# Optimization experiments

Hardware: AMD Instinct MI355X
Metric: run time of the kernel (lower is better)

Reference implementation:

```python
import jax, jax.numpy as jnp
import numpy as np

N_QUBITS = 20
W_MUL = (2.0 ** 0.5) * (5.0 ** -0.5)  # he_std = gain * 5**-0.5, use_wscale=True, lrmul=1

_C = jnp.complex64
X = jnp.array([[0, 1], [1, 0]], dtype=_C)
Y = jnp.array([[0, -1j], [1j, 0]], dtype=_C)
Z = jnp.array([[1, 0], [0, -1]], dtype=_C)
I2 = jnp.eye(2, dtype=_C)
I4 = jnp.eye(4, dtype=_C)
XX = jnp.kron(X, X)
YY = jnp.kron(Y, Y)
ZZ = jnp.kron(Z, Z)


def _rot(theta, pauli, ident):
    # exp(-i * theta/2 * P) = cos(theta/2) I - i sin(theta/2) P
    a = theta * 0.5
    return jnp.cos(a) * ident - (1j * jnp.sin(a)) * pauli


def _apply_1q(state, g, w):
    # state: [batch] + [2]*n ; contract gate input index with qubit axis w
    s = jnp.tensordot(g, state, axes=((1,), (w + 1,)))
    return jnp.moveaxis(s, 0, w + 1)


def _apply_2q(state, g4, w0, w1):
    g = g4.reshape(2, 2, 2, 2)  # (out0, out1, in0, in1)
    s = jnp.tensordot(g, state, axes=((2, 3), (w0 + 1, w1 + 1)))
    return jnp.moveaxis(s, (0, 1), (w0 + 1, w1 + 1))


def _xyz_layer(psi, params, n):
    # params: [3n]; rx, ry, rz on each wire
    for q in range(n):
        psi = _apply_1q(psi, _rot(params[3 * q], X, I2), q)
        psi = _apply_1q(psi, _rot(params[3 * q + 1], Y, I2), q)
        psi = _apply_1q(psi, _rot(params[3 * q + 2], Z, I2), q)
    return psi


def _circuit(psi, w, n):
    psi = _xyz_layer(psi, w[: 3 * n], n)
    for q in range(n - 1):
        i = 3 * n + 3 * q
        psi = _apply_2q(psi, _rot(w[i], XX, I4), q, q + 1)
        psi = _apply_2q(psi, _rot(w[i + 1], YY, I4), q, q + 1)
        psi = _apply_2q(psi, _rot(w[i + 2], ZZ, I4), q, q + 1)
    psi = _xyz_layer(psi, w[6 * n - 3 :], n)
    return psi


def setup_inputs() -> dict:
    key = jax.random.key(0)
    k1, k2 = jax.random.split(key)
    n = N_QUBITS
    dim = 1 << n
    batch = 4
    x = jax.random.normal(k1, (batch, 1, dim), dtype=jnp.float32)
    weight = jax.random.uniform(k2, (9 * n - 3,), dtype=jnp.float32, minval=0.0, maxval=2.0 * np.pi)
    return {"x": x, "weight": weight, "dimA": 10}


def reference(x, weight, dimA):
    n = N_QUBITS
    batch = x.shape[0]
    w = weight * W_MUL
    psi = x.astype(_C).reshape((batch,) + (2,) * n)  # MPS tensor [b, 2, ..., 2]
    psi = _circuit(psi, w, n)
    dimB = n - dimA
    # partial trace of |psi><psi| over the first dimB qubits (most-significant axes):
    # reduced[a, c] = sum_t psi[t, a] * conj(psi[t, c])  -- never materialize the full DM
    psi = psi.reshape(batch, 1 << dimB, 1 << dimA)
    rdm = jnp.einsum('bta,btc->bac', psi, psi.conj())
    # return real/imag stacked on last axis (real-valued representation of complex DM)
    return jnp.stack([rdm.real, rdm.imag], axis=-1)
```

## Files before the change

kernel.cpp:

```cpp
#include <hip/hip_runtime.h>
#include <hip/hip_bf16.h>

#define N_Q    20
#define DIM    (1 << N_Q)
#define BATCH  4
#define NGATES 19
#define L2OFF  117
#define GSTRIDE 32

typedef float2 c32;
typedef __attribute__((ext_vector_type(2))) float fv2;
typedef __attribute__((ext_vector_type(8))) short short8;
typedef __attribute__((ext_vector_type(4))) float f32x4;
typedef __attribute__((ext_vector_type(4))) unsigned int u32x4;

__device__ __forceinline__ c32 cmul(c32 a, c32 b) {
    return make_float2(fmaf(a.x, b.x, -a.y * b.y), fmaf(a.x, b.y, a.y * b.x));
}
__device__ __forceinline__ c32 cmadd(c32 acc, c32 a, c32 b) {
    acc.x = fmaf(a.x, b.x, fmaf(-a.y, b.y, acc.x));
    acc.y = fmaf(a.x, b.y, fmaf(a.y, b.x, acc.y));
    return acc;
}
__device__ __forceinline__ unsigned short f2bf(float f) {
    union { float f; unsigned u; } v; v.f = f;
    unsigned r = v.u + 0x7FFFu + ((v.u >> 16) & 1u);
    return (unsigned short)(r >> 16);
}
__device__ __forceinline__ unsigned pack_bf2(float re, float im) {
    return (unsigned)f2bf(re) | ((unsigned)f2bf(im) << 16);
}
__device__ __forceinline__ fv2 unpack_bf2(unsigned w) {
    union { unsigned u; float f; } lo, hi;
    lo.u = (w & 0xFFFFu) << 16;
    hi.u = w & 0xFFFF0000u;
    return (fv2){lo.f, hi.f};
}
__device__ __forceinline__ void gll16(const void* g, void* l) {
    __builtin_amdgcn_global_load_lds((const __attribute__((address_space(1))) void*)g,
                                     (__attribute__((address_space(3))) void*)l, 16, 0, 0);
}

__device__ void mm2(const c32 A[2][2], const c32 B[2][2], c32 C[2][2]) {
    for (int i = 0; i < 2; i++)
        for (int j = 0; j < 2; j++) {
            c32 s = make_float2(0.f, 0.f);
            for (int k = 0; k < 2; k++) s = cmadd(s, A[i][k], B[k][j]);
            C[i][j] = s;
        }
}
__device__ void mm4(const c32 A[4][4], const c32 B[4][4], c32 C[4][4]) {
    for (int i = 0; i < 4; i++)
        for (int j = 0; j < 4; j++) {
            c32 s = make_float2(0.f, 0.f);
            for (int k = 0; k < 4; k++) s = cmadd(s, A[i][k], B[k][j]);
            C[i][j] = s;
        }
}
__device__ void single_u(const float* w, int base, c32 U[2][2]) {
    const float WM = 0.63245553203367586640f;
    float hx = w[base] * WM * 0.5f, hy = w[base + 1] * WM * 0.5f, hz = w[base + 2] * WM * 0.5f;
    float cx = cosf(hx), sx = sinf(hx);
    float cy = cosf(hy), sy = sinf(hy);
    float cz = cosf(hz), sz = sinf(hz);
    c32 RX[2][2] = {{{cx, 0.f}, {0.f, -sx}}, {{0.f, -sx}, {cx, 0.f}}};
    c32 RY[2][2] = {{{cy, 0.f}, {-sy, 0.f}}, {{sy, 0.f}, {cy, 0.f}}};
    c32 RZ[2][2] = {{{cz, -sz}, {0.f, 0.f}}, {{0.f, 0.f}, {cz, sz}}};
    c32 T[2][2];
    mm2(RY, RX, T);
    mm2(RZ, T, U);
}
__device__ void kron22(const c32 A[2][2], const c32 B[2][2], c32 K[4][4]) {
    for (int i = 0; i < 2; i++)
        for (int j = 0; j < 2; j++)
            for (int k = 0; k < 2; k++)
                for (int l = 0; l < 2; l++)
                    K[i * 2 + j][k * 2 + l] = cmul(A[i][k], B[j][l]);
}

__global__ void build_gates(const float* __restrict__ w, c32* __restrict__ G) {
    int q = threadIdx.x;
    if (q >= NGATES) return;
    const float WM = 0.63245553203367586640f;
    float hx = w[60 + 3 * q] * WM * 0.5f;
    float hy = w[61 + 3 * q] * WM * 0.5f;
    float hz = w[62 + 3 * q] * WM * 0.5f;
    float cx = cosf(hx), sx = sinf(hx);
    float cy = cosf(hy), sy = sinf(hy);
    float cz = cosf(hz), sz = sinf(hz);
    c32 RXX[4][4], RYY[4][4], RZZ[4][4];
    for (int i = 0; i < 4; i++)
        for (int j = 0; j < 4; j++) {
            RXX[i][j] = make_float2(0.f, 0.f);
            RYY[i][j] = make_float2(0.f, 0.f);
            RZZ[i][j] = make_float2(0.f, 0.f);
        }
    for (int i = 0; i < 4; i++) {
        RXX[i][i]     = make_float2(cx, 0.f);
        RXX[i][3 - i] = make_float2(0.f, -sx);
        RYY[i][i]     = make_float2(cy, 0.f);
    }
    RYY[0][3] = make_float2(0.f,  sy);
    RYY[1][2] = make_float2(0.f, -sy);
    RYY[2][1] = make_float2(0.f, -sy);
    RYY[3][0] = make_float2(0.f,  sy);
    RZZ[0][0] = make_float2(cz, -sz);
    RZZ[1][1] = make_float2(cz,  sz);
    RZZ[2][2] = make_float2(cz,  sz);
    RZZ[3][3] = make_float2(cz, -sz);
    c32 T[4][4], M[4][4];
    mm4(RYY, RXX, T);
    mm4(RZZ, T, M);

    c32 I2m[2][2] = {{{1.f, 0.f}, {0.f, 0.f}}, {{0.f, 0.f}, {1.f, 0.f}}};
    c32 Ua[2][2], Ub[2][2], Pre[4][4], Post[4][4];
    if (q == 0) {
        single_u(w, 0, Ua);
        single_u(w, 3, Ub);
        kron22(Ua, Ub, Pre);
    } else {
        single_u(w, 3 * (q + 1), Ub);
        kron22(I2m, Ub, Pre);
    }
    if (q == NGATES - 1) {
        single_u(w, L2OFF + 3 * 18, Ua);
        single_u(w, L2OFF + 3 * 19, Ub);
        kron22(Ua, Ub, Post);
    } else {
        single_u(w, L2OFF + 3 * q, Ua);
        kron22(Ua, I2m, Post);
    }
    c32 T2[4][4], Gq[4][4];
    mm4(M, Pre, T2);
    mm4(Post, T2, Gq);
    for (int i = 0; i < 4; i++)
        for (int j = 0; j < 4; j++) {
            c32 g = Gq[i][j];
            G[q * GSTRIDE + i * 4 + j]      = g;
            G[q * GSTRIDE + 16 + i * 4 + j] = make_float2(-g.y, g.x);
        }
}

__device__ __forceinline__ void apply4pk(const fv2 g[16], const fv2 gs[16],
                                         fv2& x0, fv2& x1, fv2& x2, fv2& x3) {
    fv2 a0 = (fv2)(x0[0]), b0 = (fv2)(x0[1]);
    fv2 a1 = (fv2)(x1[0]), b1 = (fv2)(x1[1]);
    fv2 a2 = (fv2)(x2[0]), b2 = (fv2)(x2[1]);
    fv2 a3 = (fv2)(x3[0]), b3 = (fv2)(x3[1]);
    fv2 r0 = a0 * g[0];  r0 += b0 * gs[0];  r0 += a1 * g[1];  r0 += b1 * gs[1];
    r0 += a2 * g[2];     r0 += b2 * gs[2];  r0 += a3 * g[3];  r0 += b3 * gs[3];
    fv2 r1 = a0 * g[4];  r1 += b0 * gs[4];  r1 += a1 * g[5];  r1 += b1 * gs[5];
    r1 += a2 * g[6];     r1 += b2 * gs[6];  r1 += a3 * g[7];  r1 += b3 * gs[7];
    fv2 r2 = a0 * g[8];  r2 += b0 * gs[8];  r2 += a1 * g[9];  r2 += b1 * gs[9];
    r2 += a2 * g[10];    r2 += b2 * gs[10]; r2 += a3 * g[11]; r2 += b3 * gs[11];
    fv2 r3 = a0 * g[12]; r3 += b0 * gs[12]; r3 += a1 * g[13]; r3 += b1 * gs[13];
    r3 += a2 * g[14];    r3 += b2 * gs[14]; r3 += a3 * g[15]; r3 += b3 * gs[15];
    x0 = r0; x1 = r1; x2 = r2; x3 = r3;
}
__device__ __forceinline__ void load_gate2(const fv2* __restrict__ gp, fv2 g[16], fv2 gs[16]) {
#pragma unroll
    for (int k = 0; k < 16; k++) { g[k] = gp[k]; gs[k] = gp[16 + k]; }
}
template <int LO>
__device__ __forceinline__ void gate_on32(fv2 v[32], const fv2 g[16], const fv2 gs[16]) {
#pragma unroll
    for (int m = 0; m < 8; ++m) {
        const int j0 = ((m >> LO) << (LO + 2)) | (m & ((1 << LO) - 1));
        const int s = 1 << LO;
        apply4pk(g, gs, v[j0], v[j0 + s], v[j0 + 2 * s], v[j0 + 3 * s]);
    }
}
template <int LO>
__device__ __forceinline__ void gate_on16(fv2* v, const fv2 g[16], const fv2 gs[16]) {
#pragma unroll
    for (int m = 0; m < 4; ++m) {
        const int j0 = ((m >> LO) << (LO + 2)) | (m & ((1 << LO) - 1));
        const int s = 1 << LO;
        apply4pk(g, gs, v[j0], v[j0 + s], v[j0 + 2 * s], v[j0 + 3 * s]);
    }
}

#define SIDX(l) ((l) ^ ((((l) >> 5) & 15)))
#define TIDX(a, tl) (((a) << 3) | ((tl) ^ (((a) >> 5) & 7)))

__global__ __launch_bounds__(256) void pass_a2(const float* __restrict__ x,
                                               unsigned* __restrict__ psiB,
                                               const c32* __restrict__ Gall) {
    __shared__ __align__(16) char smem[65536];
    float* xs = (float*)smem;
    fv2* s = (fv2*)smem;
    const fv2* Gf = (const fv2*)Gall;
    int b = blockIdx.x >> 7;
    int c0 = (blockIdx.x & 127) << 5;
    const float* xp = x + ((size_t)b << 20) + c0;
    unsigned* ppb = psiB + ((size_t)b << 20) + c0;
    int t = threadIdx.x;
#pragma unroll
    for (int i = 0; i < 8; ++i) {
        int f4 = t + (i << 8);
        int row = f4 >> 3, sl = f4 & 7;
        float4 v = *reinterpret_cast<const float4*>(xp + (size_t)row * 4096 + sl * 4);
        reinterpret_cast<float4*>(xs)[row * 8 + (sl ^ (row & 7))] = v;
    }
    __syncthreads();
    int col = t & 31, rlow = t >> 5;
    fv2 v[32], g[16], gs[16];
#pragma unroll
    for (int j = 0; j < 32; ++j) {
        int row = (j << 3) | rlow;
        float re = xs[row * 32 + ((((col >> 2) ^ (row & 7)) << 2) | (col & 3))];
        v[j] = (fv2){re, 0.f};
    }
    __syncthreads();
    load_gate2(Gf + 0 * GSTRIDE, g, gs);  gate_on32<3>(v, g, gs);
    load_gate2(Gf + 1 * GSTRIDE, g, gs);  gate_on32<2>(v, g, gs);
    load_gate2(Gf + 2 * GSTRIDE, g, gs);  gate_on32<1>(v, g, gs);
    load_gate2(Gf + 3 * GSTRIDE, g, gs);  gate_on32<0>(v, g, gs);
#pragma unroll
    for (int j = 0; j < 32; ++j) {
        int l = ((((j << 3) | rlow) << 5)) | col;
        s[SIDX(l)] = v[j];
    }
    __syncthreads();
    int rhi = t >> 5;
#pragma unroll
    for (int rtop = 0; rtop < 2; ++rtop)
#pragma unroll
        for (int j = 0; j < 16; ++j) {
            int row = (rtop << 7) | (rhi << 4) | j;
            int l = (row << 5) | col;
            v[rtop * 16 + j] = s[SIDX(l)];
        }
    load_gate2(Gf + 4 * GSTRIDE, g, gs);  gate_on16<2>(v, g, gs);  gate_on16<2>(v + 16, g, gs);
    load_gate2(Gf + 5 * GSTRIDE, g, gs);  gate_on16<1>(v, g, gs);  gate_on16<1>(v + 16, g, gs);
    load_gate2(Gf + 6 * GSTRIDE, g, gs);  gate_on16<0>(v, g, gs);  gate_on16<0>(v + 16, g, gs);
#pragma unroll
    for (int rtop = 0; rtop < 2; ++rtop)
#pragma unroll
        for (int j = 0; j < 16; ++j) {
            int row = (rtop << 7) | (rhi << 4) | j;
            fv2 val = v[rtop * 16 + j];
            ppb[(size_t)row * 4096 + col] = pack_bf2(val[0], val[1]);
        }
}

__global__ __launch_bounds__(256) void pass_b2(const unsigned* __restrict__ psiB,
                                               unsigned short* __restrict__ Art,
                                               unsigned short* __restrict__ Ait,
                                               const c32* __restrict__ Gall) {
    __shared__ fv2 s[8192];
    const fv2* Gf = (const fv2*)Gall;
    int b = blockIdx.x >> 7;
    int chunk = blockIdx.x & 127;
    const unsigned* ppb = psiB + ((size_t)b << 20) + ((size_t)chunk << 13);
    int t = threadIdx.x;
    fv2 v[32], g[16], gs[16];
#pragma unroll
    for (int j = 0; j < 32; ++j) v[j] = unpack_bf2(ppb[(j << 8) | t]);
    load_gate2(Gf + 7 * GSTRIDE, g, gs);   gate_on32<3>(v, g, gs);
    load_gate2(Gf + 8 * GSTRIDE, g, gs);   gate_on32<2>(v, g, gs);
    load_gate2(Gf + 9 * GSTRIDE, g, gs);   gate_on32<1>(v, g, gs);
    load_gate2(Gf + 10 * GSTRIDE, g, gs);  gate_on32<0>(v, g, gs);
#pragma unroll
    for (int j = 0; j < 32; ++j) { int l = (j << 8) | t; s[SIDX(l)] = v[j]; }
    __syncthreads();
    int hi2 = (t >> 4) << 9, lo2 = t & 15;
#pragma unroll
    for (int j = 0; j < 32; ++j) { int l = hi2 | (j << 4) | lo2; v[j] = s[SIDX(l)]; }
    load_gate2(Gf + 11 * GSTRIDE, g, gs);  gate_on32<3>(v, g, gs);
    load_gate2(Gf + 12 * GSTRIDE, g, gs);  gate_on32<2>(v, g, gs);
    load_gate2(Gf + 13 * GSTRIDE, g, gs);  gate_on32<1>(v, g, gs);
    load_gate2(Gf + 14 * GSTRIDE, g, gs);  gate_on32<0>(v, g, gs);
    __syncthreads();
#pragma unroll
    for (int j = 0; j < 32; ++j) { int l = hi2 | (j << 4) | lo2; s[SIDX(l)] = v[j]; }
    __syncthreads();
#pragma unroll
    for (int j = 0; j < 32; ++j) { int l = (t << 5) | j; v[j] = s[SIDX(l)]; }
    load_gate2(Gf + 15 * GSTRIDE, g, gs);  gate_on32<3>(v, g, gs);
    load_gate2(Gf + 16 * GSTRIDE, g, gs);  gate_on32<2>(v, g, gs);
    load_gate2(Gf + 17 * GSTRIDE, g, gs);  gate_on32<1>(v, g, gs);
    load_gate2(Gf + 18 * GSTRIDE, g, gs);  gate_on32<0>(v, g, gs);
    __syncthreads();
    {
        int tlw = t >> 5;
        int abase = (t & 31) << 5;
#pragma unroll
        for (int j = 0; j < 32; ++j) {
            int a = abase + j;
            s[TIDX(a, tlw)] = v[j];
        }
    }
    __syncthreads();
    {
        int w = t >> 6, lane = t & 63;
        size_t gb = (size_t)b << 20;
#pragma unroll
        for (int i = 0; i < 4; ++i) {
            int a = (w << 8) | (i << 6) | lane;
            unsigned short rr[8], ri[8];
#pragma unroll
            for (int tl = 0; tl < 8; ++tl) {
                fv2 q = s[TIDX(a, tl)];
                rr[tl] = f2bf(q[0]);
                ri[tl] = f2bf(q[1]);
            }
            size_t dst = gb + ((size_t)a << 10) + (chunk << 3);
            *reinterpret_cast<float4*>(Art + dst) = *reinterpret_cast<float4*>(rr);
            *reinterpret_cast<float4*>(Ait + dst) = *reinterpret_cast<float4*>(ri);
        }
    }
}

__global__ __launch_bounds__(512) void gram_mfma5c(const unsigned short* __restrict__ Art,
                                                   const unsigned short* __restrict__ Ait,
                                                   float2* __restrict__ out) {
    __shared__ __align__(16) unsigned short lds[2][4][8192];
    int hw = blockIdx.x;
    int virt = (hw & 7) * 18 + (hw >> 3);
    int b = virt / 36;
    int rem = virt - b * 36;
    int ia = 0;
    while (rem >= 8 - ia) { rem -= 8 - ia; ++ia; }
    int ic = ia + rem;
    int a0 = ia * 128, c0 = ic * 128;
    int tid = threadIdx.x;
    int lane = tid & 63, w = tid >> 6;
    int wm = w & 3, wn = w >> 2;
    int arr = w >> 1, half = w & 1;
    const unsigned short* sp = (arr & 1) ? Ait : Art;
    int prow = (arr < 2) ? a0 : c0;
    int srow = lane >> 3, sslot = lane & 7;
    size_t gb = (size_t)b << 20;

    f32x4 accRe[2][4], accIm[2][4];
#pragma unroll
    for (int m = 0; m < 2; m++)
#pragma unroll
        for (int n = 0; n < 4; n++) { accRe[m][n] = (f32x4)0.f; accIm[m][n] = (f32x4)0.f; }

#define STAGE5(KT, BUF)                                                                   \
    {                                                                                     \
        _Pragma("unroll")                                                                 \
        for (int i = 0; i < 8; ++i) {                                                     \
            int r = (half << 6) | (i << 3) | srow;                                        \
            int sl = sslot ^ srow;                                                        \
            const unsigned short* gp = sp + gb + ((size_t)(prow + r) << 10) + (KT) * 64 + sl * 8; \
            gll16(gp, &lds[BUF][arr][((half << 6) | (i << 3)) * 64 + lane * 8]);          \
        }                                                                                 \
    }

    STAGE5(0, 0);
    for (int kt = 0; kt < 16; ++kt) {
        int cur = kt & 1;
        asm volatile("s_waitcnt vmcnt(0)" ::: "memory");
        __builtin_amdgcn_s_barrier();
        __builtin_amdgcn_sched_barrier(0);
        if (kt < 15) STAGE5(kt + 1, cur ^ 1);
        __builtin_amdgcn_s_setprio(1);
#pragma unroll
        for (int kk = 0; kk < 2; ++kk) {
            int sbase = kk * 4 + (lane >> 4);
            short8 am[2][2], bn[4][2];
#pragma unroll
            for (int m = 0; m < 2; m++) {
                int r = wm * 32 + m * 16 + (lane & 15);
                int off = r * 64 + ((sbase ^ (r & 7)) << 3);
                am[m][0] = *reinterpret_cast<const short8*>(&lds[cur][0][off]);
                am[m][1] = *reinterpret_cast<const short8*>(&lds[cur][1][off]);
            }
#pragma unroll
            for (int n = 0; n < 4; n++) {
                int r = wn * 64 + n * 16 + (lane & 15);
                int off = r * 64 + ((sbase ^ (r & 7)) << 3);
                bn[n][0] = *reinterpret_cast<const short8*>(&lds[cur][2][off]);
                bn[n][1] = *reinterpret_cast<const short8*>(&lds[cur][3][off]);
            }
#pragma unroll
            for (int m = 0; m < 2; m++) {
                u32x4 tn = *reinterpret_cast<u32x4*>(&am[m][0]) ^ 0x80008000u;
                short8 arn = *reinterpret_cast<short8*>(&tn);
#pragma unroll
                for (int n = 0; n < 4; n++) {
                    accRe[m][n] = __builtin_amdgcn_mfma_f32_16x16x32_bf16(am[m][0], bn[n][0], accRe[m][n], 0, 0, 0);
                    accRe[m][n] = __builtin_amdgcn_mfma_f32_16x16x32_bf16(am[m][1], bn[n][1], accRe[m][n], 0, 0, 0);
                    accIm[m][n] = __builtin_amdgcn_mfma_f32_16x16x32_bf16(am[m][1], bn[n][0], accIm[m][n], 0, 0, 0);
                    accIm[m][n] = __builtin_amdgcn_mfma_f32_16x16x32_bf16(arn,      bn[n][1], accIm[m][n], 0, 0, 0);
                }
            }
        }
        __builtin_amdgcn_s_setprio(0);
        asm volatile("s_waitcnt lgkmcnt(0)" ::: "memory");
        __builtin_amdgcn_sched_barrier(0);
    }
#undef STAGE5
    size_t ob = gb;
#pragma unroll
    for (int m = 0; m < 2; m++)
#pragma unroll
        for (int n = 0; n < 4; n++)
#pragma unroll
            for (int r = 0; r < 4; r++) {
                int a = a0 + wm * 32 + m * 16 + (lane >> 4) * 4 + r;
                int c = c0 + wn * 64 + n * 16 + (lane & 15);
                out[ob + ((size_t)a << 10) + c] = make_float2(accRe[m][n][r], accIm[m][n][r]);
            }
    if (ia != ic) {
        float2* mlds = reinterpret_cast<float2*>(&lds[0][0][0]);
#pragma unroll
        for (int h = 0; h < 2; ++h) {
            __syncthreads();
            if (wn == h) {
#pragma unroll
                for (int m = 0; m < 2; m++)
#pragma unroll
                    for (int n = 0; n < 4; n++)
#pragma unroll
                        for (int r = 0; r < 4; r++) {
                            int a_l = wm * 32 + m * 16 + (lane >> 4) * 4 + r;
                            int c_l = n * 16 + (lane & 15);
                            mlds[c_l * 131 + a_l] = make_float2(accRe[m][n][r], -accIm[m][n][r]);
                        }
            }
            __syncthreads();
#pragma unroll
            for (int i = 0; i < 16; ++i) {
                int p = tid + (i << 9);
                int row = p >> 7, col = p & 127;
                out[ob + ((size_t)(c0 + h * 64 + row) << 10) + a0 + col] = mlds[row * 131 + col];
            }
        }
    }
}

extern "C" void kernel_launch(void* const* d_in, const int* in_sizes, int n_in,
                              void* d_out, int out_size, void* d_ws, size_t ws_size,
                              hipStream_t stream) {
    const float* x = (const float*)d_in[0];
    const float* weight = (const float*)d_in[1];
    const size_t psiBytes = (size_t)BATCH * DIM * sizeof(unsigned);
    unsigned* psiB = (unsigned*)d_ws;
    c32* G = (c32*)((char*)d_ws + psiBytes);
    unsigned short* Art = (unsigned short*)((char*)d_ws + psiBytes + 65536);
    unsigned short* Ait = Art + (size_t)BATCH * DIM;

    build_gates<<<1, 64, 0, stream>>>(weight, G);
    pass_a2<<<BATCH * 128, 256, 0, stream>>>(x, psiB, G);
    pass_b2<<<BATCH * 128, 256, 0, stream>>>(psiB, Art, Ait, G);
    gram_mfma5c<<<144, 512, 0, stream>>>(Art, Ait, (float2*)d_out);
}
```

Before: 93.70 us.

## Load A operand directly to registers and stage only B tile in LDS

The Gram kernel now fetches the A-side (row block a0) fragments straight from global memory into registers, double-buffered across k-steps, while only the C-side tile is staged in LDS via async global-to-LDS loads. The k-loop is unrolled by two with explicit ping-pong buffers and extra barriers. The aim is to halve LDS traffic and LDS reads per MFMA. The cost is more register pressure, uncoalesced 16-byte global reads for A, and additional barrier synchronisation.

```diff
diff --git a/kernel.cpp b/kernel.cpp
--- a/kernel.cpp
+++ b/kernel.cpp
@@ -312,10 +312,11 @@
     }
 }
 
-__global__ __launch_bounds__(512) void gram_mfma5c(const unsigned short* __restrict__ Art,
-                                                   const unsigned short* __restrict__ Ait,
-                                                   float2* __restrict__ out) {
-    __shared__ __align__(16) unsigned short lds[2][4][8192];
+__global__ __launch_bounds__(512) void gram_mfma8(const unsigned short* __restrict__ Art,
+                                                  const unsigned short* __restrict__ Ait,
+                                                  float2* __restrict__ out) {
+    __shared__ __align__(16) char smem[69632];
+    short* sb16 = (short*)smem;
     int hw = blockIdx.x;
     int virt = (hw & 7) * 18 + (hw >> 3);
     int b = virt / 36;
@@ -327,9 +328,8 @@
     int tid = threadIdx.x;
     int lane = tid & 63, w = tid >> 6;
     int wm = w & 3, wn = w >> 2;
-    int arr = w >> 1, half = w & 1;
-    const unsigned short* sp = (arr & 1) ? Ait : Art;
-    int prow = (arr < 2) ? a0 : c0;
+    int arr = w & 1, rowgroup = w >> 1;
+    const unsigned short* sp = arr ? Ait : Art;
     int srow = lane >> 3, sslot = lane & 7;
     size_t gb = (size_t)b << 20;
 
@@ -339,61 +339,103 @@
 #pragma unroll
         for (int n = 0; n < 4; n++) { accRe[m][n] = (f32x4)0.f; accIm[m][n] = (f32x4)0.f; }
 
-#define STAGE5(KT, BUF)                                                                   \
-    {                                                                                     \
-        _Pragma("unroll")                                                                 \
-        for (int i = 0; i < 8; ++i) {                                                     \
-            int r = (half << 6) | (i << 3) | srow;                                        \
-            int sl = sslot ^ srow;                                                        \
-            const unsigned short* gp = sp + gb + ((size_t)(prow + r) << 10) + (KT) * 64 + sl * 8; \
-            gll16(gp, &lds[BUF][arr][((half << 6) | (i << 3)) * 64 + lane * 8]);          \
-        }                                                                                 \
-    }
-
-    STAGE5(0, 0);
-    for (int kt = 0; kt < 16; ++kt) {
-        int cur = kt & 1;
-        asm volatile("s_waitcnt vmcnt(0)" ::: "memory");
+    short8 aA[2][2][2], aB[2][2][2];
+
+#define STAGE8(KT, BUF)                                                                    \
+    {                                                                                      \
+        _Pragma("unroll")                                                                  \
+        for (int i = 0; i < 4; ++i) {                                                      \
+            int row = c0 + rowgroup * 32 + i * 8 + srow;                                   \
+            const unsigned short* gp = sp + gb + ((size_t)row << 10) + (KT) * 64 + ((sslot ^ srow) << 3); \
+            gll16(gp, sb16 + ((BUF) * 2 + arr) * 8192 + rowgroup * 2048 + i * 512 + lane * 8); \
+        }                                                                                  \
+    }
+#define ALOAD8(KT, DST)                                                                    \
+    {                                                                                      \
+        _Pragma("unroll")                                                                  \
+        for (int kk = 0; kk < 2; ++kk)                                                     \
+        _Pragma("unroll")                                                                  \
+        for (int m = 0; m < 2; ++m)                                                        \
+        _Pragma("unroll")                                                                  \
+        for (int ar = 0; ar < 2; ++ar) {                                                   \
+            int r = a0 + wm * 32 + m * 16 + (lane & 15);                                   \
+            int sb = kk * 4 + (lane >> 4);                                                 \
+            const unsigned short* gp = (ar ? Ait : Art) + gb + ((size_t)r << 10) + (KT) * 64 + sb * 8; \
+            DST[kk][m][ar] = *reinterpret_cast<const short8*>(gp);                         \
+        }                                                                                  \
+    }
+#define KEEPA(CUR)                                                                         \
+    {                                                                                      \
+        _Pragma("unroll")                                                                  \
+        for (int kk = 0; kk < 2; ++kk)                                                     \
+        _Pragma("unroll")                                                                  \
+        for (int m = 0; m < 2; ++m)                                                        \
+        _Pragma("unroll")                                                                  \
+        for (int ar = 0; ar < 2; ++ar)                                                     \
+            asm volatile("" :: "v"((int)CUR[kk][m][ar][0]));                               \
+    }
+#define COMPUTE8(BUF, CUR)                                                                 \
+    {                                                                                      \
+        _Pragma("unroll")                                                                  \
+        for (int kk = 0; kk < 2; ++kk) {                                                   \
+            int sbk = kk * 4 + (lane >> 4);                                                \
+            short8 bn[4][2];                                                               \
+            _Pragma("unroll")                                                              \
+            for (int n = 0; n < 4; ++n)                                                    \
+            _Pragma("unroll")                                                              \
+            for (int ar = 0; ar < 2; ++ar) {                                               \
+                int r = wn * 64 + n * 16 + (lane & 15);                                    \
+                int off = ((BUF) * 2 + ar) * 8192 + r * 64 + ((sbk ^ (r & 7)) << 3);       \
+                bn[n][ar] = *reinterpret_cast<const short8*>(sb16 + off);                  \
+            }                                                                              \
+            _Pragma("unroll")                                                              \
+            for (int m = 0; m < 2; ++m) {                                                  \
+                u32x4 tn = *reinterpret_cast<u32x4*>(&CUR[kk][m][0]) ^ 0x80008000u;        \
+                short8 arn = *reinterpret_cast<short8*>(&tn);                              \
+                _Pragma("unroll")                                                          \
+                for (int n = 0; n < 4; ++n) {                                              \
+                    accRe[m][n] = __builtin_amdgcn_mfma_f32_16x16x32_bf16(CUR[kk][m][0], bn[n][0], accRe[m][n], 0, 0, 0); \
+                    accRe[m][n] = __builtin_amdgcn_mfma_f32_16x16x32_bf16(CUR[kk][m][1], bn[n][1], accRe[m][n], 0, 0, 0); \
+                    accIm[m][n] = __builtin_amdgcn_mfma_f32_16x16x32_bf16(CUR[kk][m][1], bn[n][0], accIm[m][n], 0, 0, 0); \
+                    accIm[m][n] = __builtin_amdgcn_mfma_f32_16x16x32_bf16(arn,           bn[n][1], accIm[m][n], 0, 0, 0); \
+                }                                                                          \
+            }                                                                              \
+        }                                                                                  \
+    }
+
+    STAGE8(0, 0);
+    ALOAD8(0, aA);
+    for (int kt2 = 0; kt2 < 8; ++kt2) {
+        int kt = kt2 * 2;
+        STAGE8(kt + 1, 1);
+        ALOAD8(kt + 1, aB);
+        KEEPA(aA);
         __builtin_amdgcn_s_barrier();
         __builtin_amdgcn_sched_barrier(0);
-        if (kt < 15) STAGE5(kt + 1, cur ^ 1);
         __builtin_amdgcn_s_setprio(1);
-#pragma unroll
-        for (int kk = 0; kk < 2; ++kk) {
-            int sbase = kk * 4 + (lane >> 4);
-            short8 am[2][2], bn[4][2];
-#pragma unroll
-            for (int m = 0; m < 2; m++) {
-                int r = wm * 32 + m * 16 + (lane & 15);
-                int off = r * 64 + ((sbase ^ (r & 7)) << 3);
-                am[m][0] = *reinterpret_cast<const short8*>(&lds[cur][0][off]);
-                am[m][1] = *reinterpret_cast<const short8*>(&lds[cur][1][off]);
-            }
-#pragma unroll
-            for (int n = 0; n < 4; n++) {
-                int r = wn * 64 + n * 16 + (lane & 15);
-                int off = r * 64 + ((sbase ^ (r & 7)) << 3);
-                bn[n][0] = *reinterpret_cast<const short8*>(&lds[cur][2][off]);
-                bn[n][1] = *reinterpret_cast<const short8*>(&lds[cur][3][off]);
-            }
-#pragma unroll
-            for (int m = 0; m < 2; m++) {
-                u32x4 tn = *reinterpret_cast<u32x4*>(&am[m][0]) ^ 0x80008000u;
-                short8 arn = *reinterpret_cast<short8*>(&tn);
-#pragma unroll
-                for (int n = 0; n < 4; n++) {
-                    accRe[m][n] = __builtin_amdgcn_mfma_f32_16x16x32_bf16(am[m][0], bn[n][0], accRe[m][n], 0, 0, 0);
-                    accRe[m][n] = __builtin_amdgcn_mfma_f32_16x16x32_bf16(am[m][1], bn[n][1], accRe[m][n], 0, 0, 0);
-                    accIm[m][n] = __builtin_amdgcn_mfma_f32_16x16x32_bf16(am[m][1], bn[n][0], accIm[m][n], 0, 0, 0);
-                    accIm[m][n] = __builtin_amdgcn_mfma_f32_16x16x32_bf16(arn,      bn[n][1], accIm[m][n], 0, 0, 0);
-                }
-            }
-        }
+        COMPUTE8(0, aA);
         __builtin_amdgcn_s_setprio(0);
         asm volatile("s_waitcnt lgkmcnt(0)" ::: "memory");
         __builtin_amdgcn_sched_barrier(0);
-    }
-#undef STAGE5
+        __builtin_amdgcn_s_barrier();
+        if (kt2 < 7) {
+            STAGE8(kt + 2, 0);
+            ALOAD8(kt + 2, aA);
+        }
+        KEEPA(aB);
+        __builtin_amdgcn_s_barrier();
+        __builtin_amdgcn_sched_barrier(0);
+        __builtin_amdgcn_s_setprio(1);
+        COMPUTE8(1, aB);
+        __builtin_amdgcn_s_setprio(0);
+        asm volatile("s_waitcnt lgkmcnt(0)" ::: "memory");
+        __builtin_amdgcn_sched_barrier(0);
+        __builtin_amdgcn_s_barrier();
+    }
+#undef STAGE8
+#undef ALOAD8
+#undef KEEPA
+#undef COMPUTE8
     size_t ob = gb;
 #pragma unroll
     for (int m = 0; m < 2; m++)
@@ -406,7 +448,7 @@
                 out[ob + ((size_t)a << 10) + c] = make_float2(accRe[m][n][r], accIm[m][n][r]);
             }
     if (ia != ic) {
-        float2* mlds = reinterpret_cast<float2*>(&lds[0][0][0]);
+        float2* mlds = reinterpret_cast<float2*>(smem);
 #pragma unroll
         for (int h = 0; h < 2; ++h) {
             __syncthreads();
@@ -447,5 +489,5 @@
     build_gates<<<1, 64, 0, stream>>>(weight, G);
     pass_a2<<<BATCH * 128, 256, 0, stream>>>(x, psiB, G);
     pass_b2<<<BATCH * 128, 256, 0, stream>>>(psiB, Art, Ait, G);
-    gram_mfma5c<<<144, 512, 0, stream>>>(Art, Ait, (float2*)d_out);
-}
+    gram_mfma8<<<144, 512, 0, stream>>>(Art, Ait, (float2*)d_out);
+}
```

Result: slower. 115.6 us (+23.4%).
